# Optimization experiments

Measured on AMD Instinct MI355X. Metric: run time of the kernel, lower is better.

Reference implementation:

```python
import jax, jax.numpy as jnp
import numpy as np

B, H, W, D, C = 2, 16, 16, 16, 128
UNITS = 128
BN_EPS = 1e-3  # keras BatchNormalization default epsilon


def setup_inputs() -> dict:
    key = jax.random.key(0)
    ks = jax.random.split(key, 12)
    lim = np.sqrt(3.0 / C)  # VarianceScaling(1.0, fan_avg, uniform)
    inp = {
        "x": jax.random.normal(ks[0], (B, H, W, D, C), dtype=jnp.float32),
        "gamma": jnp.ones((C,), jnp.float32),
        "beta": jnp.zeros((C,), jnp.float32),
        "moving_mean": jax.random.normal(ks[1], (C,), jnp.float32) * 0.1,
        "moving_var": jnp.ones((C,), jnp.float32) + 0.1 * jax.random.uniform(ks[2], (C,)),
        "Wq": jax.random.uniform(ks[3], (C, UNITS), jnp.float32, -lim, lim),
        "bq": jnp.zeros((UNITS,), jnp.float32),
        "Wk": jax.random.uniform(ks[4], (C, UNITS), jnp.float32, -lim, lim),
        "bk": jnp.zeros((UNITS,), jnp.float32),
        "Wv": jax.random.uniform(ks[5], (C, UNITS), jnp.float32, -lim, lim),
        "bv": jnp.zeros((UNITS,), jnp.float32),
        # proj uses kernel_init(0.0) -> effectively ~0; use tiny scale to keep grads nonzero
        "Wp": jax.random.uniform(ks[6], (UNITS, UNITS), jnp.float32, -1e-5, 1e-5),
        "bp": jnp.zeros((UNITS,), jnp.float32),
    }
    return inp


def reference(x, gamma, beta, moving_mean, moving_var, Wq, bq, Wk, bk, Wv, bv, Wp, bp):
    # BatchNormalization (inference mode): per-channel affine normalization
    xn = (x - moving_mean) * jax.lax.rsqrt(moving_var + BN_EPS) * gamma + beta
    b, h, w, d, c = xn.shape
    n = h * w * d
    scale = jnp.asarray(UNITS, jnp.float32) ** -0.5
    q = (xn @ Wq + bq).reshape(b, n, UNITS)
    k = (xn @ Wk + bk).reshape(b, n, UNITS)
    v = (xn @ Wv + bv).reshape(b, n, UNITS)
    # full self-attention over flattened 3D spatial dims: [b, n, n] scores
    attn = jax.nn.softmax(jnp.einsum('bnc,bmc->bnm', q, k) * scale, axis=-1)
    proj = jnp.einsum('bnm,bmc->bnc', attn, v).reshape(b, h, w, d, UNITS)
    proj = proj @ Wp + bp
    return xn + proj
```

## Files before the change

kernel.cpp:

```cpp
#include <hip/hip_runtime.h>
#include <hip/hip_bf16.h>

using bh8     = __attribute__((ext_vector_type(8))) short;
using floatx4 = __attribute__((ext_vector_type(4))) float;

#define MFMA16 __builtin_amdgcn_mfma_f32_16x16x32_bf16

__device__ __forceinline__ float b2f(short s) {
    union { unsigned u; float f; } v; v.u = ((unsigned)(unsigned short)s) << 16; return v.f;
}
__device__ __forceinline__ short f2b(float f) {
    union { float f; unsigned u; } v; v.f = f;
    unsigned r = (v.u + 0x7fffu + ((v.u >> 16) & 1u)) >> 16;
    return (short)r;
}
__device__ __forceinline__ float ldf(const void* p, int i, bool f32) {
    return f32 ? ((const float*)p)[i] : b2f(((const short*)p)[i]);
}
__device__ __forceinline__ bool detect_f32(const void* gamma) {
    return ((*(const unsigned*)gamma) & 0xFFFFu) == 0u;
}
__device__ __forceinline__ void gl2lds16(const short* g, short* l) {
    __builtin_amdgcn_global_load_lds(
        (const __attribute__((address_space(1))) void*)g,
        (__attribute__((address_space(3))) void*)l, 16, 0, 0);
}

#define LDW 136

__global__ __launch_bounds__(256) void k_bn_qkv(
    const void* __restrict__ xp,
    const void* __restrict__ gp, const void* __restrict__ bep,
    const void* __restrict__ mmp, const void* __restrict__ mvp,
    const void* __restrict__ Wqp, const void* __restrict__ bqp,
    const void* __restrict__ Wkp, const void* __restrict__ bkp,
    const void* __restrict__ Wvp, const void* __restrict__ bvp,
    short* __restrict__ Qo, short* __restrict__ Ko, short* __restrict__ Vt)
{
    __shared__ float sS[128], sT[128];
    __shared__ __align__(16) short Wt[128 * LDW];
    const bool f32 = detect_f32(gp);
    const int tid = threadIdx.x, wave = tid >> 6, lane = tid & 63;
    const int lq = lane >> 4, lr = lane & 15;
    const int g = blockIdx.x >> 6;
    const int tile = blockIdx.x & 63;
    const int row0 = tile * 128 + wave * 32;

    if (tid < 128) {
        float ga = ldf(gp, tid, f32), be = ldf(bep, tid, f32);
        float mm = ldf(mmp, tid, f32), mv = ldf(mvp, tid, f32);
        float s = ga * rsqrtf(mv + 1e-3f);
        sS[tid] = s;
        sT[tid] = be - mm * s;
    }

    const void* W  = (g == 0) ? Wqp : ((g == 1) ? Wkp : Wvp);
    const void* bb = (g == 0) ? bqp : ((g == 1) ? bkp : bvp);

    if (f32) {
        for (int it = 0; it < 16; ++it) {
            int f = (it * 256 + tid) * 4;
            int c = f >> 7, u = f & 127;
            floatx4 wv = *(const floatx4*)((const float*)W + f);
            #pragma unroll
            for (int jj = 0; jj < 4; ++jj) {
                int j = (jj + (tid >> 1)) & 3;
                Wt[(u + j) * LDW + c] = f2b(wv[j]);
            }
        }
    } else {
        for (int it = 0; it < 8; ++it) {
            int f = (it * 256 + tid) * 8;
            int c = f >> 7, u = f & 127;
            bh8 wv = *(const bh8*)((const short*)W + f);
            #pragma unroll
            for (int jj = 0; jj < 8; ++jj) {
                int j = (jj + tid) & 7;
                Wt[(u + j) * LDW + c] = wv[j];
            }
        }
    }
    __syncthreads();

    bh8 a[2][4];
    #pragma unroll
    for (int rt = 0; rt < 2; ++rt)
        #pragma unroll
        for (int ks = 0; ks < 4; ++ks) {
            int c0 = ks * 32 + lq * 8;
            floatx4 s0 = *(const floatx4*)(&sS[c0]), s1 = *(const floatx4*)(&sS[c0 + 4]);
            floatx4 t0 = *(const floatx4*)(&sT[c0]), t1 = *(const floatx4*)(&sT[c0 + 4]);
            bh8 af;
            if (f32) {
                const float* xr = (const float*)xp + (size_t)(row0 + rt * 16 + lr) * 128 + c0;
                floatx4 x0 = *(const floatx4*)xr, x1 = *(const floatx4*)(xr + 4);
                #pragma unroll
                for (int j = 0; j < 4; ++j) {
                    af[j]     = f2b(x0[j] * s0[j] + t0[j]);
                    af[j + 4] = f2b(x1[j] * s1[j] + t1[j]);
                }
            } else {
                bh8 xv = *(const bh8*)((const short*)xp + (size_t)(row0 + rt * 16 + lr) * 128 + c0);
                #pragma unroll
                for (int j = 0; j < 4; ++j) {
                    af[j]     = f2b(b2f(xv[j]) * s0[j] + t0[j]);
                    af[j + 4] = f2b(b2f(xv[j + 4]) * s1[j] + t1[j]);
                }
            }
            a[rt][ks] = af;
        }

    floatx4 acc[2][8] = {};
    #pragma unroll
    for (int ks = 0; ks < 4; ++ks)
        #pragma unroll
        for (int t = 0; t < 8; ++t) {
            bh8 b = *(const bh8*)(&Wt[(t * 16 + lr) * LDW + ks * 32 + lq * 8]);
            #pragma unroll
            for (int rt = 0; rt < 2; ++rt)
                acc[rt][t] = MFMA16(a[rt][ks], b, acc[rt][t], 0, 0, 0);
        }

    if (g < 2) {
        #pragma unroll
        for (int t = 0; t < 8; ++t) {
            int u = t * 16 + lr;
            float bias = ldf(bb, u, f32);
            #pragma unroll
            for (int rt = 0; rt < 2; ++rt)
                #pragma unroll
                for (int r = 0; r < 4; ++r) {
                    int grow = row0 + rt * 16 + lq * 4 + r;
                    short vb = f2b(acc[rt][t][r] + bias);
                    if (g == 0) Qo[(size_t)grow * 128 + u] = vb;
                    else        Ko[(size_t)grow * 128 + u] = vb;
                }
        }
    } else {
        __syncthreads();
        short* sVt = Wt;
        #pragma unroll
        for (int t = 0; t < 8; ++t) {
            int u = t * 16 + lr;
            float bias = ldf(bb, u, f32);
            #pragma unroll
            for (int rt = 0; rt < 2; ++rt)
                #pragma unroll
                for (int r = 0; r < 4; ++r) {
                    int n = wave * 32 + rt * 16 + lq * 4 + r;
                    sVt[u * LDW + n] = f2b(acc[rt][t][r] + bias);
                }
        }
        __syncthreads();
        int u = tid >> 1, nh = tid & 1;
        int grow0 = tile * 128 + nh * 64;
        int bsb = grow0 >> 12, nn = grow0 & 4095;
        short* dst = Vt + (size_t)bsb * 128 * 4096 + (size_t)u * 4096 + nn;
        #pragma unroll
        for (int j = 0; j < 8; ++j)
            *(bh8*)(dst + j * 8) = *(const bh8*)(&sVt[u * LDW + nh * 64 + j * 8]);
    }
}

#define PLDA 40

__global__ __launch_bounds__(256, 2) void k_attn(
    const short* __restrict__ Qg, const short* __restrict__ Kg,
    const short* __restrict__ Vtg, short* __restrict__ Op,
    float* __restrict__ Lq)
{
    __shared__ __align__(16) short sK[2][32 * 128];
    __shared__ __align__(16) short sV[2][128 * 32];
    __shared__ __align__(16) short sP[4][32 * PLDA];

    const int tid = threadIdx.x, wave = tid >> 6, lane = tid & 63;
    const int lq = lane >> 4, lr = lane & 15;
    const int qt = blockIdx.x >> 3, kq = blockIdx.x & 7;
    const int mq = qt * 128, bs = mq >> 12, key0q = kq * 512;
    const short* Kb = Kg + (size_t)bs * 4096 * 128;
    const short* Vb = Vtg + (size_t)bs * 128 * 4096;
    const int qrow0 = mq + wave * 32;

    bh8 aq[2][4];
    #pragma unroll
    for (int rt = 0; rt < 2; ++rt)
        #pragma unroll
        for (int ks = 0; ks < 4; ++ks)
            aq[rt][ks] = *(const bh8*)(Qg + (size_t)(qrow0 + rt * 16 + lr) * 128 + ks * 32 + lq * 8);

    const int kKey = lane >> 4, kCh = lane & 15;
    const int vU   = lane >> 2, vCh = lane & 3;

    floatx4 accO[2][8] = {};
    float lsum[2][4] = {};
    const float c2 = 0.12751743f;
    const float m2 = 11.541560f;
    short* Pw = &sP[wave][0];

    #pragma unroll
    for (int rd = 0; rd < 2; ++rd) {
        int key = wave * 8 + rd * 4 + kKey;
        gl2lds16(Kb + (size_t)(key0q + key) * 128 + ((kCh ^ (key & 7)) << 3),
                 &sK[0][(wave * 8 + rd * 4) * 128]);
    }
    #pragma unroll
    for (int rd = 0; rd < 2; ++rd) {
        int u = wave * 32 + rd * 16 + vU;
        gl2lds16(Vb + (size_t)u * 4096 + key0q + ((vCh ^ ((u >> 1) & 3)) << 3),
                 &sV[0][(wave * 32 + rd * 16) * 32]);
    }
    __syncthreads();

    for (int it = 0; it < 16; ++it) {
        const int p = it & 1;
        if (it < 15) {
            const int key1 = key0q + (it + 1) * 32;
            #pragma unroll
            for (int rd = 0; rd < 2; ++rd) {
                int key = wave * 8 + rd * 4 + kKey;
                gl2lds16(Kb + (size_t)(key1 + key) * 128 + ((kCh ^ (key & 7)) << 3),
                         &sK[p ^ 1][(wave * 8 + rd * 4) * 128]);
            }
            #pragma unroll
            for (int rd = 0; rd < 2; ++rd) {
                int u = wave * 32 + rd * 16 + vU;
                gl2lds16(Vb + (size_t)u * 4096 + key1 + ((vCh ^ ((u >> 1) & 3)) << 3),
                         &sV[p ^ 1][(wave * 32 + rd * 16) * 32]);
            }
        }

        const short* sKp = &sK[p][0];
        const short* sVp = &sV[p][0];

        floatx4 s[2][2];
        #pragma unroll
        for (int rt = 0; rt < 2; ++rt)
            #pragma unroll
            for (int t = 0; t < 2; ++t)
                s[rt][t] = floatx4{};
        #pragma unroll
        for (int t = 0; t < 2; ++t)
            #pragma unroll
            for (int ks = 0; ks < 4; ++ks) {
                bh8 b = *(const bh8*)(&sKp[(t * 16 + lr) * 128 +
                                           (((ks * 4 + lq) ^ (lr & 7)) << 3)]);
                #pragma unroll
                for (int rt = 0; rt < 2; ++rt)
                    s[rt][t] = MFMA16(aq[rt][ks], b, s[rt][t], 0, 0, 0);
            }

        #pragma unroll
        for (int rt = 0; rt < 2; ++rt)
            #pragma unroll
            for (int t = 0; t < 2; ++t)
                #pragma unroll
                for (int r = 0; r < 4; ++r) {
                    float e = exp2f(fmaf(s[rt][t][r], c2, -m2));
                    s[rt][t][r] = e;
                    lsum[rt][r] += e;
                }

        #pragma unroll
        for (int rt = 0; rt < 2; ++rt)
            #pragma unroll
            for (int t = 0; t < 2; ++t)
                #pragma unroll
                for (int r = 0; r < 4; ++r)
                    Pw[(rt * 16 + lq * 4 + r) * PLDA + t * 16 + lr] = f2b(s[rt][t][r]);

        bh8 ap[2];
        #pragma unroll
        for (int rt = 0; rt < 2; ++rt)
            ap[rt] = *(const bh8*)(&Pw[(rt * 16 + lr) * PLDA + lq * 8]);

        #pragma unroll
        for (int t = 0; t < 8; ++t) {
            int u = t * 16 + lr;
            bh8 b = *(const bh8*)(&sVp[u * 32 + ((lq ^ ((lr >> 1) & 3)) << 3)]);
            #pragma unroll
            for (int rt = 0; rt < 2; ++rt)
                accO[rt][t] = MFMA16(ap[rt], b, accO[rt][t], 0, 0, 0);
        }
        if (it < 15) __syncthreads();
    }

    #pragma unroll
    for (int rt = 0; rt < 2; ++rt)
        #pragma unroll
        for (int r = 0; r < 4; ++r) {
            float v = lsum[rt][r];
            v += __shfl_xor(v, 1, 16);
            v += __shfl_xor(v, 2, 16);
            v += __shfl_xor(v, 4, 16);
            v += __shfl_xor(v, 8, 16);
            lsum[rt][r] = v;
        }
    if (lr == 0) {
        #pragma unroll
        for (int rt = 0; rt < 2; ++rt)
            #pragma unroll
            for (int r = 0; r < 4; ++r)
                Lq[(size_t)kq * 8192 + qrow0 + rt * 16 + lq * 4 + r] = lsum[rt][r];
    }
    short* Ob = Op + (size_t)kq * 8192 * 128;
    #pragma unroll
    for (int rt = 0; rt < 2; ++rt)
        #pragma unroll
        for (int t = 0; t < 8; ++t)
            #pragma unroll
            for (int r = 0; r < 4; ++r)
                Ob[(size_t)(qrow0 + rt * 16 + lq * 4 + r) * 128 + t * 16 + lr]
                    = f2b(accO[rt][t][r]);
}

__global__ __launch_bounds__(256) void k_proj(
    const short* __restrict__ Op, const float* __restrict__ Lq,
    const void* __restrict__ Wpp, const void* __restrict__ bpp,
    const void* __restrict__ xp,
    const void* __restrict__ gp, const void* __restrict__ bep,
    const void* __restrict__ mmp, const void* __restrict__ mvp,
    void* __restrict__ outp)
{
    __shared__ float sS[128], sT[128];
    __shared__ __align__(16) short Wt[64 * LDW];
    __shared__ __align__(16) short sO[32 * LDW];
    const bool f32 = detect_f32(gp);
    const int tid = threadIdx.x, wave = tid >> 6, lane = tid & 63;
    const int lq = lane >> 4, lr = lane & 15;
    const int uh = blockIdx.x & 1;
    const int tile = blockIdx.x >> 1;
    const int row0 = tile * 32;
    const int rh = wave >> 1, us = wave & 1;

    if (tid < 128) {
        float ga = ldf(gp, tid, f32), be = ldf(bep, tid, f32);
        float mm = ldf(mmp, tid, f32), mv = ldf(mvp, tid, f32);
        float s = ga * rsqrtf(mv + 1e-3f);
        sS[tid] = s;
        sT[tid] = be - mm * s;
    }

    if (f32) {
        for (int it = 0; it < 8; ++it) {
            int f = (it * 256 + tid) * 4;
            int c = f >> 6, ul = f & 63;
            floatx4 wv = *(const floatx4*)((const float*)Wpp + (size_t)c * 128 + uh * 64 + ul);
            #pragma unroll
            for (int jj = 0; jj < 4; ++jj) {
                int j = (jj + (tid >> 1)) & 3;
                Wt[(ul + j) * LDW + c] = f2b(wv[j]);
            }
        }
    } else {
        for (int it = 0; it < 4; ++it) {
            int f = (it * 256 + tid) * 8;
            int c = f >> 6, ul = f & 63;
            bh8 wv = *(const bh8*)((const short*)Wpp + (size_t)c * 128 + uh * 64 + ul);
            #pragma unroll
            for (int jj = 0; jj < 8; ++jj) {
                int j = (jj + tid) & 7;
                Wt[(ul + j) * LDW + c] = wv[j];
            }
        }
    }

    #pragma unroll
    for (int e = 0; e < 2; ++e) {
        int f = (e * 256 + tid) * 8;
        int row = f >> 7, c = f & 127;
        int grow = row0 + row;
        float L = 0.f;
        #pragma unroll
        for (int w = 0; w < 8; ++w) L += Lq[(size_t)w * 8192 + grow];
        float invL = 1.0f / L;
        float sum[8] = {};
        #pragma unroll
        for (int w = 0; w < 8; ++w) {
            bh8 p = *(const bh8*)(Op + (size_t)w * 8192 * 128 + (size_t)grow * 128 + c);
            #pragma unroll
            for (int j = 0; j < 8; ++j) sum[j] += b2f(p[j]);
        }
        bh8 o;
        #pragma unroll
        for (int j = 0; j < 8; ++j) o[j] = f2b(sum[j] * invL);
        *(bh8*)(&sO[row * LDW + c]) = o;
    }
    __syncthreads();

    bh8 a[4];
    #pragma unroll
    for (int ks = 0; ks < 4; ++ks)
        a[ks] = *(const bh8*)(&sO[(rh * 16 + lr) * LDW + ks * 32 + lq * 8]);

    floatx4 acc[2] = {};
    #pragma unroll
    for (int ks = 0; ks < 4; ++ks)
        #pragma unroll
        for (int t = 0; t < 2; ++t) {
            bh8 b = *(const bh8*)(&Wt[(us * 32 + t * 16 + lr) * LDW + ks * 32 + lq * 8]);
            acc[t] = MFMA16(a[ks], b, acc[t], 0, 0, 0);
        }

    #pragma unroll
    for (int t = 0; t < 2; ++t) {
        int u = uh * 64 + us * 32 + t * 16 + lr;
        float bias = ldf(bpp, u, f32);
        float su = sS[u], tu = sT[u];
        #pragma unroll
        for (int r = 0; r < 4; ++r) {
            int grow = row0 + rh * 16 + lq * 4 + r;
            float xnv = ldf(xp, grow * 128 + u, f32) * su + tu;
            float v = acc[t][r] + bias + xnv;
            size_t idx = (size_t)grow * 128 + u;
            if (f32) ((float*)outp)[idx] = v;
            else     ((short*)outp)[idx] = f2b(v);
        }
    }
}

extern "C" void kernel_launch(void* const* d_in, const int* in_sizes, int n_in,
                              void* d_out, int out_size, void* d_ws, size_t ws_size,
                              hipStream_t stream)
{
    const void* x     = d_in[0];
    const void* gamma = d_in[1];
    const void* beta  = d_in[2];
    const void* mmean = d_in[3];
    const void* mvar  = d_in[4];
    const void* Wq    = d_in[5];
    const void* bq    = d_in[6];
    const void* Wk    = d_in[7];
    const void* bk    = d_in[8];
    const void* Wv    = d_in[9];
    const void* bv    = d_in[10];
    const void* Wp    = d_in[11];
    const void* bp    = d_in[12];

    char* ws = (char*)d_ws;
    const size_t MB = 1024u * 1024u;
    short* Q     = (short*)(ws + 0 * MB);
    short* K     = (short*)(ws + 2 * MB);
    short* Vt    = (short*)(ws + 4 * MB);
    short* Opart = (short*)(ws + 6 * MB);
    float* Lsum  = (float*)(ws + 22 * MB);

    k_bn_qkv<<<192, 256, 0, stream>>>(x, gamma, beta, mmean, mvar,
                                      Wq, bq, Wk, bk, Wv, bv, Q, K, Vt);
    k_attn<<<512, 256, 0, stream>>>(Q, K, Vt, Opart, Lsum);
    k_proj<<<512, 256, 0, stream>>>(Opart, Lsum, Wp, bp, x,
                                    gamma, beta, mmean, mvar, d_out);
}
```

Measured before the change: 134.6 us.

## Transpose attention score tile for packed P stores; retile projection kernel

The attention kernel swaps the MFMA operands so the score tile comes out transposed. Each lane then holds four consecutive keys of one query row. That lets the exp'd probabilities be packed into bf16 pairs and written to LDS as 8-byte stores instead of sixteen scalar short stores. It also cuts the per-lane row-sum state and the final reduction to two cross-row shuffles. The projection kernel now handles 16 rows per block against the full 128-wide Wp, with a min-blocks launch bound. This trades a larger per-block transpose of Wp for fewer redundant O/L reduction reads.

```diff
diff --git a/kernel.cpp b/kernel.cpp
--- a/kernel.cpp
+++ b/kernel.cpp
@@ -3,6 +3,7 @@
 
 using bh8     = __attribute__((ext_vector_type(8))) short;
 using floatx4 = __attribute__((ext_vector_type(4))) float;
+using uintx2  = __attribute__((ext_vector_type(2))) unsigned;
 
 #define MFMA16 __builtin_amdgcn_mfma_f32_16x16x32_bf16
 
@@ -13,6 +14,11 @@
     union { float f; unsigned u; } v; v.f = f;
     unsigned r = (v.u + 0x7fffu + ((v.u >> 16) & 1u)) >> 16;
     return (short)r;
+}
+__device__ __forceinline__ unsigned pk2(float a, float b) {
+    union { __hip_bfloat162 h; unsigned u; } v;
+    v.h = __float22bfloat162_rn(make_float2(a, b));
+    return v.u;
 }
 __device__ __forceinline__ float ldf(const void* p, int i, bool f32) {
     return f32 ? ((const float*)p)[i] : b2f(((const short*)p)[i]);
@@ -192,7 +198,7 @@
     const int vU   = lane >> 2, vCh = lane & 3;
 
     floatx4 accO[2][8] = {};
-    float lsum[2][4] = {};
+    float lsum[2] = {};
     const float c2 = 0.12751743f;
     const float m2 = 11.541560f;
     short* Pw = &sP[wave][0];
@@ -242,31 +248,28 @@
         for (int t = 0; t < 2; ++t)
             #pragma unroll
             for (int ks = 0; ks < 4; ++ks) {
-                bh8 b = *(const bh8*)(&sKp[(t * 16 + lr) * 128 +
-                                           (((ks * 4 + lq) ^ (lr & 7)) << 3)]);
+                bh8 kf = *(const bh8*)(&sKp[(t * 16 + lr) * 128 +
+                                            (((ks * 4 + lq) ^ (lr & 7)) << 3)]);
                 #pragma unroll
                 for (int rt = 0; rt < 2; ++rt)
-                    s[rt][t] = MFMA16(aq[rt][ks], b, s[rt][t], 0, 0, 0);
+                    s[rt][t] = MFMA16(kf, aq[rt][ks], s[rt][t], 0, 0, 0);
             }
 
         #pragma unroll
         for (int rt = 0; rt < 2; ++rt)
             #pragma unroll
-            for (int t = 0; t < 2; ++t)
+            for (int t = 0; t < 2; ++t) {
+                float e[4];
                 #pragma unroll
                 for (int r = 0; r < 4; ++r) {
-                    float e = exp2f(fmaf(s[rt][t][r], c2, -m2));
-                    s[rt][t][r] = e;
-                    lsum[rt][r] += e;
+                    e[r] = exp2f(fmaf(s[rt][t][r], c2, -m2));
+                    lsum[rt] += e[r];
                 }
-
-        #pragma unroll
-        for (int rt = 0; rt < 2; ++rt)
-            #pragma unroll
-            for (int t = 0; t < 2; ++t)
-                #pragma unroll
-                for (int r = 0; r < 4; ++r)
-                    Pw[(rt * 16 + lq * 4 + r) * PLDA + t * 16 + lr] = f2b(s[rt][t][r]);
+                uintx2 pw;
+                pw[0] = pk2(e[0], e[1]);
+                pw[1] = pk2(e[2], e[3]);
+                *(uintx2*)(&Pw[(rt * 16 + lr) * PLDA + t * 16 + lq * 4]) = pw;
+            }
 
         bh8 ap[2];
         #pragma unroll
@@ -285,22 +288,12 @@
     }
 
     #pragma unroll
-    for (int rt = 0; rt < 2; ++rt)
-        #pragma unroll
-        for (int r = 0; r < 4; ++r) {
-            float v = lsum[rt][r];
-            v += __shfl_xor(v, 1, 16);
-            v += __shfl_xor(v, 2, 16);
-            v += __shfl_xor(v, 4, 16);
-            v += __shfl_xor(v, 8, 16);
-            lsum[rt][r] = v;
-        }
-    if (lr == 0) {
-        #pragma unroll
-        for (int rt = 0; rt < 2; ++rt)
-            #pragma unroll
-            for (int r = 0; r < 4; ++r)
-                Lq[(size_t)kq * 8192 + qrow0 + rt * 16 + lq * 4 + r] = lsum[rt][r];
+    for (int rt = 0; rt < 2; ++rt) {
+        float v = lsum[rt];
+        v += __shfl_xor(v, 16, 64);
+        v += __shfl_xor(v, 32, 64);
+        if (lane < 16)
+            Lq[(size_t)kq * 8192 + qrow0 + rt * 16 + lr] = v;
     }
     short* Ob = Op + (size_t)kq * 8192 * 128;
     #pragma unroll
@@ -313,7 +306,7 @@
                     = f2b(accO[rt][t][r]);
 }
 
-__global__ __launch_bounds__(256) void k_proj(
+__global__ __launch_bounds__(256, 2) void k_proj(
     const short* __restrict__ Op, const float* __restrict__ Lq,
     const void* __restrict__ Wpp, const void* __restrict__ bpp,
     const void* __restrict__ xp,
@@ -322,15 +315,12 @@
     void* __restrict__ outp)
 {
     __shared__ float sS[128], sT[128];
-    __shared__ __align__(16) short Wt[64 * LDW];
-    __shared__ __align__(16) short sO[32 * LDW];
+    __shared__ __align__(16) short Wt[128 * LDW];
+    __shared__ __align__(16) short sO[16 * LDW];
     const bool f32 = detect_f32(gp);
     const int tid = threadIdx.x, wave = tid >> 6, lane = tid & 63;
     const int lq = lane >> 4, lr = lane & 15;
-    const int uh = blockIdx.x & 1;
-    const int tile = blockIdx.x >> 1;
-    const int row0 = tile * 32;
-    const int rh = wave >> 1, us = wave & 1;
+    const int row0 = blockIdx.x * 16;
 
     if (tid < 128) {
         float ga = ldf(gp, tid, f32), be = ldf(bep, tid, f32);
@@ -341,32 +331,31 @@
     }
 
     if (f32) {
-        for (int it = 0; it < 8; ++it) {
+        for (int it = 0; it < 16; ++it) {
             int f = (it * 256 + tid) * 4;
-            int c = f >> 6, ul = f & 63;
-            floatx4 wv = *(const floatx4*)((const float*)Wpp + (size_t)c * 128 + uh * 64 + ul);
+            int c = f >> 7, u = f & 127;
+            floatx4 wv = *(const floatx4*)((const float*)Wpp + f);
             #pragma unroll
             for (int jj = 0; jj < 4; ++jj) {
                 int j = (jj + (tid >> 1)) & 3;
-                Wt[(ul + j) * LDW + c] = f2b(wv[j]);
+                Wt[(u + j) * LDW + c] = f2b(wv[j]);
             }
         }
     } else {
-        for (int it = 0; it < 4; ++it) {
+        for (int it = 0; it < 8; ++it) {
             int f = (it * 256 + tid) * 8;
-            int c = f >> 6, ul = f & 63;
-            bh8 wv = *(const bh8*)((const short*)Wpp + (size_t)c * 128 + uh * 64 + ul);
+            int c = f >> 7, u = f & 127;
+            bh8 wv = *(const bh8*)((const short*)Wpp + f);
             #pragma unroll
             for (int jj = 0; jj < 8; ++jj) {
                 int j = (jj + tid) & 7;
-                Wt[(ul + j) * LDW + c] = wv[j];
-            }
-        }
-    }
-
-    #pragma unroll
-    for (int e = 0; e < 2; ++e) {
-        int f = (e * 256 + tid) * 8;
+                Wt[(u + j) * LDW + c] = wv[j];
+            }
+        }
+    }
+
+    {
+        int f = tid * 8;
         int row = f >> 7, c = f & 127;
         int grow = row0 + row;
         float L = 0.f;
@@ -390,27 +379,27 @@
     bh8 a[4];
     #pragma unroll
     for (int ks = 0; ks < 4; ++ks)
-        a[ks] = *(const bh8*)(&sO[(rh * 16 + lr) * LDW + ks * 32 + lq * 8]);
+        a[ks] = *(const bh8*)(&sO[lr * LDW + ks * 32 + lq * 8]);
 
     floatx4 acc[2] = {};
     #pragma unroll
     for (int ks = 0; ks < 4; ++ks)
         #pragma unroll
-        for (int t = 0; t < 2; ++t) {
-            bh8 b = *(const bh8*)(&Wt[(us * 32 + t * 16 + lr) * LDW + ks * 32 + lq * 8]);
-            acc[t] = MFMA16(a[ks], b, acc[t], 0, 0, 0);
-        }
-
-    #pragma unroll
-    for (int t = 0; t < 2; ++t) {
-        int u = uh * 64 + us * 32 + t * 16 + lr;
+        for (int tt = 0; tt < 2; ++tt) {
+            bh8 b = *(const bh8*)(&Wt[(wave * 32 + tt * 16 + lr) * LDW + ks * 32 + lq * 8]);
+            acc[tt] = MFMA16(a[ks], b, acc[tt], 0, 0, 0);
+        }
+
+    #pragma unroll
+    for (int tt = 0; tt < 2; ++tt) {
+        int u = wave * 32 + tt * 16 + lr;
         float bias = ldf(bpp, u, f32);
         float su = sS[u], tu = sT[u];
         #pragma unroll
         for (int r = 0; r < 4; ++r) {
-            int grow = row0 + rh * 16 + lq * 4 + r;
+            int grow = row0 + lq * 4 + r;
             float xnv = ldf(xp, grow * 128 + u, f32) * su + tu;
-            float v = acc[t][r] + bias + xnv;
+            float v = acc[tt][r] + bias + xnv;
             size_t idx = (size_t)grow * 128 + u;
             if (f32) ((float*)outp)[idx] = v;
             else     ((short*)outp)[idx] = f2b(v);
```

Result: faster. 130.0 us (-3.4%).
